# Kernel tuning notes

Hardware: AMD Instinct MI355X
Metric: run time of the kernel (lower is better)

## Reference

```python
import jax, jax.numpy as jnp
import numpy as np

B, T, D = 8, 2048, 256  # batch, time segments, feature dim (a_dim=v_dim=hidden=out=256)
EPS = 1e-8


def _layer_norm(x, g, b, eps=1e-6):
    m = jnp.mean(x, axis=-1, keepdims=True)
    v = jnp.var(x, axis=-1, keepdims=True)
    return (x - m) * jax.lax.rsqrt(v + eps) * g + b


def setup_inputs() -> dict:
    key = jax.random.key(0)
    ks = jax.random.split(key, 9)
    xav = lambda k: jax.random.uniform(k, (D, D), jnp.float32, -1.0, 1.0) * np.sqrt(6.0 / (D + D))
    return {
        "a_fea": jax.random.normal(ks[0], (B, T, D), jnp.float32),
        "v_fea": jax.random.normal(ks[1], (B, T, D), jnp.float32),
        "thr_val": jnp.float32(0.099),
        "Wv1": xav(ks[2]), "Wv2": xav(ks[3]), "Wvfc": xav(ks[4]),
        "Wa1": xav(ks[5]), "Wa2": xav(ks[6]), "Wafc": xav(ks[7]),
        "ln_g": jnp.ones((D,), jnp.float32),
        "ln_b": jnp.zeros((D,), jnp.float32),
    }


def reference(a_fea, v_fea, thr_val, Wv1, Wv2, Wvfc, Wa1, Wa2, Wafc, ln_g, ln_b):
    relu = jax.nn.relu
    # branch projections (dropout is identity at eval); torch Linear: x @ W.T
    v1 = relu(jnp.einsum('btd,hd->bth', v_fea, Wv1))
    v2 = relu(jnp.einsum('btd,hd->bth', v_fea, Wv2))
    a1 = relu(jnp.einsum('btd,hd->bth', a_fea, Wa1))
    a2 = relu(jnp.einsum('btd,hd->bth', a_fea, Wa2))

    d = v2.shape[-1]
    # scaled cross-modal scores, ReLU'd  [B, Tv, Ta]
    beta_va = relu(jnp.einsum('btd,bsd->bts', v2, a1) / jnp.sqrt(jnp.float32(d)))
    # a->v scores taken BEFORE row-normalization of beta_va (as in torch code)
    beta_av = jnp.transpose(beta_va, (0, 2, 1))

    time = beta_va.shape[-1]
    thr = thr_val * 10.0 / time

    # normalize -> threshold sparsify -> renormalize (v attends to a)
    bn_va = beta_va / (jnp.sum(beta_va, axis=-1, keepdims=True) + EPS)
    g_va = jnp.where(bn_va > thr, bn_va, 0.0)
    g_va = g_va / (jnp.sum(g_va, axis=-1, keepdims=True) + EPS)

    # same for a attends to v
    bn_av = beta_av / (jnp.sum(beta_av, axis=-1, keepdims=True) + EPS)
    g_av = jnp.where(bn_av > thr, bn_av, 0.0)
    g_av = g_av / (jnp.sum(g_av, axis=-1, keepdims=True) + EPS)

    # vectorized form of the diagonal selection double-loop (batch element 0)
    pred = (jnp.diagonal(g_av[0]) > 0).astype(jnp.float32)  # [T]

    a_pos = jnp.einsum('bts,bsd->btd', g_va, a2)
    v_psp = v_fea + a_pos
    v_pos = jnp.einsum('bts,bsd->btd', g_av, v1)
    a_psp = a_fea + v_pos

    v_psp = _layer_norm(relu(jnp.einsum('btd,od->bto', v_psp, Wvfc)), ln_g, ln_b)
    a_psp = _layer_norm(relu(jnp.einsum('btd,od->bto', a_psp, Wafc)), ln_g, ln_b)
    a_v_fuse = 0.5 * (v_psp + a_psp)
    return a_v_fuse, v_psp, a_psp, pred
```

## Files before the change

kernel.cpp:

```cpp
#include <hip/hip_runtime.h>
#include <math.h>

#define TT 2048
#define DD 256
#define NBATCH 8
#define EPSF 1e-8f

typedef unsigned short u16;
typedef __attribute__((ext_vector_type(8))) short short8;
typedef __attribute__((ext_vector_type(4))) float f32x4;

__device__ __forceinline__ u16 f2bf(float x) {
    unsigned int u = __builtin_bit_cast(unsigned int, x);
    u += 0x7fffu + ((u >> 16) & 1u);
    return (u16)(u >> 16);
}
__device__ __forceinline__ float bf2f(u16 h) {
    return __builtin_bit_cast(float, (unsigned int)h << 16);
}

__device__ __forceinline__ int frag_dst(int row, int k) {
    return (((row >> 4) * 4 + (k >> 3)) * 16 + (row & 15)) * 8 + (k & 7);
}

__device__ __forceinline__ int swz(int i) { return i ^ ((i >> 2) & 32); }

template<int BR>
__device__ __forceinline__ void stage_tile(const u16* __restrict__ g, u16* s,
                                           int row0, int k0, int ldk, int tid)
{
    #pragma unroll
    for (int i = 0; i < BR / 64; ++i) {
        const int c = tid + 256 * i;
        const int row = c >> 2, q = c & 3;
        *(int4*)(s + swz(frag_dst(row, q * 8))) =
            *(const int4*)(g + (long)(row0 + row) * ldk + k0 + q * 8);
    }
}

__global__ __launch_bounds__(512)
void proj_kernel(const u16* __restrict__ vfh, const u16* __restrict__ vfl,
                 const u16* __restrict__ afh, const u16* __restrict__ afl,
                 const u16* __restrict__ Wsp,
                 u16* __restrict__ v2h, u16* __restrict__ v2l,
                 u16* __restrict__ a1h, u16* __restrict__ a1l,
                 u16* __restrict__ v1T, u16* __restrict__ a2T)
{
    const int zz = blockIdx.z;
    const u16* Ah = (zz == 1 || zz == 3) ? afh : vfh;
    const u16* Al = (zz == 1 || zz == 3) ? afl : vfl;
    const int widx = (zz == 0) ? 2 : (zz == 1) ? 4 : (zz == 2) ? 0 : 6;
    const u16* Bh = Wsp + widx * DD * DD;
    const u16* Bl = Bh + DD * DD;
    const bool split = zz < 2;
    u16* Oh = (zz == 0) ? v2h : a1h;
    u16* Ol = (zz == 0) ? v2l : a1l;
    u16* OT = (zz == 2) ? v1T : a2T;

    __shared__ __align__(16) u16 Ah_s[128 * 32], Al_s[128 * 32];
    __shared__ __align__(16) u16 Bh_s[64 * 32], Bl_s[64 * 32];
    const int m0 = blockIdx.y * 128, n0 = blockIdx.x * 64;
    const int tid = threadIdx.x, lane = tid & 63, w = tid >> 6;
    const int wy = w >> 2, wx = w & 3;
    f32x4 acc[4] = {};

    const int prow = tid >> 2, pq = tid & 3;
    const int dA = swz(frag_dst(prow, pq * 8));
    const u16* gAh = Ah + (long)(m0 + prow) * DD + pq * 8;
    const u16* gAl = Al + (long)(m0 + prow) * DD + pq * 8;
    const int brow = (tid & 255) >> 2, bq = tid & 3;
    const int dB = swz(frag_dst(brow, bq * 8));
    const u16* gB = ((tid < 256) ? Bh : Bl) + (long)(n0 + brow) * DD + bq * 8;
    u16* sB = (tid < 256) ? Bh_s : Bl_s;

    int4 rAh = *(const int4*)(gAh);
    int4 rAl = *(const int4*)(gAl);
    int4 rB  = *(const int4*)(gB);

    for (int k0 = 0; k0 < DD; k0 += 32) {
        *(int4*)(Ah_s + dA) = rAh;
        *(int4*)(Al_s + dA) = rAl;
        *(int4*)(sB + dB)   = rB;
        __syncthreads();
        const int kn = (k0 + 32 < DD) ? k0 + 32 : 0;
        rAh = *(const int4*)(gAh + kn);
        rAl = *(const int4*)(gAl + kn);
        rB  = *(const int4*)(gB + kn);
        short8 ah[4], al[4], bh, bl;
        #pragma unroll
        for (int i = 0; i < 4; ++i) {
            ah[i] = *(const short8*)(Ah_s + swz(((wy * 4 + i) * 64 + lane) * 8));
            al[i] = *(const short8*)(Al_s + swz(((wy * 4 + i) * 64 + lane) * 8));
        }
        bh = *(const short8*)(Bh_s + swz((wx * 64 + lane) * 8));
        bl = *(const short8*)(Bl_s + swz((wx * 64 + lane) * 8));
        #pragma unroll
        for (int i = 0; i < 4; ++i) {
            acc[i] = __builtin_amdgcn_mfma_f32_16x16x32_bf16(ah[i], bl, acc[i], 0, 0, 0);
            acc[i] = __builtin_amdgcn_mfma_f32_16x16x32_bf16(al[i], bh, acc[i], 0, 0, 0);
            acc[i] = __builtin_amdgcn_mfma_f32_16x16x32_bf16(ah[i], bh, acc[i], 0, 0, 0);
        }
        __syncthreads();
    }
    const int quad = lane >> 4, col = lane & 15;
    const int c = n0 + wx * 16 + col;
    #pragma unroll
    for (int i = 0; i < 4; ++i) {
        const int rbase = m0 + wy * 64 + i * 16 + quad * 4;
        if (split) {
            #pragma unroll
            for (int r = 0; r < 4; ++r) {
                const float v = fmaxf(acc[i][r], 0.f);
                const u16 h = f2bf(v);
                Oh[(long)(rbase + r) * DD + c] = h;
                Ol[(long)(rbase + r) * DD + c] = f2bf(v - bf2f(h));
            }
        } else {
            short4 pk;
            pk.x = (short)f2bf(fmaxf(acc[i][0], 0.f));
            pk.y = (short)f2bf(fmaxf(acc[i][1], 0.f));
            pk.z = (short)f2bf(fmaxf(acc[i][2], 0.f));
            pk.w = (short)f2bf(fmaxf(acc[i][3], 0.f));
            const int b = rbase >> 11, t = rbase & (TT - 1);
            *(short4*)(OT + ((long)b * DD + c) * TT + t) = pk;
        }
    }
}

__global__ __launch_bounds__(512)
void score_kernel(const u16* __restrict__ v2h, const u16* __restrict__ v2l,
                  const u16* __restrict__ a1h, const u16* __restrict__ a1l,
                  u16* __restrict__ beta, u16* __restrict__ betaT,
                  float* __restrict__ rs, float* __restrict__ cs)
{
    __shared__ __align__(16) u16 S[128 * 136];
    u16* Ah_s = S;
    u16* Al_s = S + 4096;
    u16* Bh_s = S + 8192;
    u16* Bl_s = S + 12288;
    const int z = blockIdx.z;
    const int m0 = blockIdx.y * 128, n0 = blockIdx.x * 128;
    const int tid = threadIdx.x, lane = tid & 63, w = tid >> 6;
    const int wy = w >> 2, wx = w & 3;
    const long zoff = (long)z * TT * DD;
    f32x4 acc[4][2] = {};

    const int prow = tid >> 2, pq = tid & 3;
    const int d0 = swz(frag_dst(prow, pq * 8));
    const u16* gAh = v2h + zoff + (long)(m0 + prow) * DD + pq * 8;
    const u16* gAl = v2l + zoff + (long)(m0 + prow) * DD + pq * 8;
    const u16* gBh = a1h + zoff + (long)(n0 + prow) * DD + pq * 8;
    const u16* gBl = a1l + zoff + (long)(n0 + prow) * DD + pq * 8;

    int4 rAh = *(const int4*)(gAh);
    int4 rAl = *(const int4*)(gAl);
    int4 rBh = *(const int4*)(gBh);
    int4 rBl = *(const int4*)(gBl);

    for (int k0 = 0; k0 < DD; k0 += 32) {
        *(int4*)(Ah_s + d0) = rAh;
        *(int4*)(Al_s + d0) = rAl;
        *(int4*)(Bh_s + d0) = rBh;
        *(int4*)(Bl_s + d0) = rBl;
        __syncthreads();
        const int kn = (k0 + 32 < DD) ? k0 + 32 : 0;
        rAh = *(const int4*)(gAh + kn);
        rAl = *(const int4*)(gAl + kn);
        rBh = *(const int4*)(gBh + kn);
        rBl = *(const int4*)(gBl + kn);
        short8 ah[4], al[4], bh[2], bl[2];
        #pragma unroll
        for (int i = 0; i < 4; ++i) {
            ah[i] = *(const short8*)(Ah_s + swz(((wy * 4 + i) * 64 + lane) * 8));
            al[i] = *(const short8*)(Al_s + swz(((wy * 4 + i) * 64 + lane) * 8));
        }
        #pragma unroll
        for (int j = 0; j < 2; ++j) {
            bh[j] = *(const short8*)(Bh_s + swz(((wx * 2 + j) * 64 + lane) * 8));
            bl[j] = *(const short8*)(Bl_s + swz(((wx * 2 + j) * 64 + lane) * 8));
        }
        #pragma unroll
        for (int i = 0; i < 4; ++i)
            #pragma unroll
            for (int j = 0; j < 2; ++j) {
                acc[i][j] = __builtin_amdgcn_mfma_f32_16x16x32_bf16(ah[i], bl[j], acc[i][j], 0, 0, 0);
                acc[i][j] = __builtin_amdgcn_mfma_f32_16x16x32_bf16(al[i], bh[j], acc[i][j], 0, 0, 0);
                acc[i][j] = __builtin_amdgcn_mfma_f32_16x16x32_bf16(ah[i], bh[j], acc[i][j], 0, 0, 0);
            }
        __syncthreads();
    }

    const int quad = lane >> 4, col = lane & 15;
    const float scale = 1.f / 16.f;
    #pragma unroll
    for (int i = 0; i < 4; ++i)
        #pragma unroll
        for (int j = 0; j < 2; ++j)
            #pragma unroll
            for (int r = 0; r < 4; ++r)
                acc[i][j][r] = fmaxf(acc[i][j][r] * scale, 0.f);

    #pragma unroll
    for (int i = 0; i < 4; ++i) {
        const int rl = (wy * 4 + i) * 16 + quad * 4;
        #pragma unroll
        for (int j = 0; j < 2; ++j) {
            const int cl = (wx * 2 + j) * 16 + col;
            #pragma unroll
            for (int r = 0; r < 4; ++r)
                S[(rl + r) * 136 + cl] = f2bf(acc[i][j][r]);
        }
    }
    __syncthreads();
    #pragma unroll
    for (int it = 0; it < 4; ++it) {
        const int idx = tid + 512 * it;
        const int rl = idx >> 4, cq = idx & 15;
        const int4 v = *(const int4*)(S + rl * 136 + cq * 8);
        *(int4*)(beta + ((long)z * TT + m0 + rl) * TT + n0 + cq * 8) = v;
    }
    #pragma unroll
    for (int i = 0; i < 4; ++i)
        #pragma unroll
        for (int r = 0; r < 4; ++r) {
            float rp = acc[i][0][r] + acc[i][1][r];
            rp += __shfl_xor(rp, 1); rp += __shfl_xor(rp, 2);
            rp += __shfl_xor(rp, 4); rp += __shfl_xor(rp, 8);
            if (col == 0) {
                const int row = m0 + (wy * 4 + i) * 16 + quad * 4 + r;
                atomicAdd(&rs[(long)z * TT + row], rp);
            }
        }
    #pragma unroll
    for (int j = 0; j < 2; ++j) {
        float cp = 0.f;
        #pragma unroll
        for (int i = 0; i < 4; ++i)
            #pragma unroll
            for (int r = 0; r < 4; ++r) cp += acc[i][j][r];
        cp += __shfl_xor(cp, 16); cp += __shfl_xor(cp, 32);
        if (lane < 16) {
            const int c = n0 + (wx * 2 + j) * 16 + col;
            atomicAdd(&cs[(long)z * TT + c], cp);
        }
    }
    __syncthreads();
    #pragma unroll
    for (int i = 0; i < 4; ++i)
        #pragma unroll
        for (int j = 0; j < 2; ++j) {
            const int cl = (wx * 2 + j) * 16 + col;
            const int rl = (wy * 4 + i) * 16 + quad * 4;
            short4 pk;
            pk.x = (short)f2bf(acc[i][j][0]);
            pk.y = (short)f2bf(acc[i][j][1]);
            pk.z = (short)f2bf(acc[i][j][2]);
            pk.w = (short)f2bf(acc[i][j][3]);
            *(short4*)(S + cl * 136 + rl) = pk;
        }
    __syncthreads();
    #pragma unroll
    for (int it = 0; it < 4; ++it) {
        const int idx = tid + 512 * it;
        const int cl = idx >> 4, tq = idx & 15;
        const int4 v = *(const int4*)(S + cl * 136 + tq * 8);
        *(int4*)(betaT + ((long)z * TT + n0 + cl) * TT + m0 + tq * 8) = v;
    }
}

__global__ __launch_bounds__(512)
void pv_kernel(const u16* __restrict__ beta, const u16* __restrict__ betaT,
               const u16* __restrict__ a2T, const u16* __restrict__ v1T,
               const float* __restrict__ rs, const float* __restrict__ cs,
               const float* __restrict__ thrp,
               u16* __restrict__ yvin, u16* __restrict__ yain)
{
    __shared__ __align__(16) u16 A_s[128 * 32], B_s[256 * 32];
    __shared__ float sthr[128], sA[128], ssum[128];
    const int zz = blockIdx.x;
    const int m0 = blockIdx.y * 128;
    const int z = zz & 7;
    const bool av = zz >= 8;
    const u16* P      = av ? betaT : beta;
    const u16* VT     = av ? v1T : a2T;
    const float* sums = av ? cs : rs;
    u16* outb         = av ? yain : yvin;

    const int tid = threadIdx.x, lane = tid & 63, w = tid >> 6;
    const int wy = w >> 2, wx = w & 3;
    const float thr = thrp[0] * 10.0f / (float)TT;
    if (tid < 128) {
        const float s = sums[(long)z * TT + m0 + tid];
        sA[tid] = s; sthr[tid] = thr * (s + EPSF); ssum[tid] = 0.f;
    }
    __syncthreads();
    f32x4 acc[4][4] = {};
    float rpart = 0.f;
    const int arow = tid >> 2, aq = tid & 3;
    const u16* Pp = P + ((long)z * TT + m0 + arow) * TT + aq * 8;
    const u16* V0 = VT + (long)z * DD * TT + (long)arow * TT + aq * 8;
    const u16* V1 = V0 + (long)128 * TT;
    const int da  = swz(frag_dst(arow, aq * 8));
    const int db1 = swz(frag_dst(arow + 128, aq * 8));

    int4 Ar  = *(const int4*)(Pp);
    int4 Br0 = *(const int4*)(V0);
    int4 Br1 = *(const int4*)(V1);

    for (int k0 = 0; k0 < TT; k0 += 32) {
        union { int4 v; u16 us[8]; } U;
        U.v = Ar;
        const float ct = sthr[arow];
        float ss = 0.f;
        #pragma unroll
        for (int t = 0; t < 8; ++t) {
            const float v = bf2f(U.us[t]);
            if (v > ct) ss += v; else U.us[t] = 0;
        }
        rpart += ss;
        *(int4*)(A_s + da) = U.v;
        *(int4*)(B_s + da) = Br0;
        *(int4*)(B_s + db1) = Br1;
        __syncthreads();
        const int kn = (k0 + 32 < TT) ? (k0 + 32) : k0;
        Ar  = *(const int4*)(Pp + kn);
        Br0 = *(const int4*)(V0 + kn);
        Br1 = *(const int4*)(V1 + kn);
        short8 a[4], b[4];
        #pragma unroll
        for (int i = 0; i < 4; ++i)
            a[i] = *(const short8*)(A_s + swz(((wy * 4 + i) * 64 + lane) * 8));
        #pragma unroll
        for (int j = 0; j < 4; ++j)
            b[j] = *(const short8*)(B_s + swz(((wx * 4 + j) * 64 + lane) * 8));
        #pragma unroll
        for (int i = 0; i < 4; ++i)
            #pragma unroll
            for (int j = 0; j < 4; ++j)
                acc[i][j] = __builtin_amdgcn_mfma_f32_16x16x32_bf16(a[i], b[j], acc[i][j], 0, 0, 0);
        __syncthreads();
    }
    atomicAdd(&ssum[arow], rpart);
    __syncthreads();

    const int quad = lane >> 4, col = lane & 15;
    #pragma unroll
    for (int i = 0; i < 4; ++i)
        #pragma unroll
        for (int j = 0; j < 4; ++j) {
            const int c = (wx * 4 + j) * 16 + col;
            #pragma unroll
            for (int r = 0; r < 4; ++r) {
                const int lrow = (wy * 4 + i) * 16 + quad * 4 + r;
                const int row = m0 + lrow;
                const float inv = 1.0f / (ssum[lrow] + EPSF * (sA[lrow] + EPSF));
                const long oidx = ((long)z * TT + row) * DD + c;
                const float v = acc[i][j][r] * inv + bf2f(outb[oidx]);
                outb[oidx] = f2bf(v);
            }
        }
}

__global__ __launch_bounds__(256)
void fc_kernel(const u16* __restrict__ Ain, const u16* __restrict__ Wb,
               u16* __restrict__ Cb)
{
    const int z = blockIdx.z;
    const u16* A = Ain + (size_t)z * (size_t)NBATCH * TT * DD;
    const u16* B = Wb + (size_t)z * DD * DD;
    u16* C = Cb + (size_t)z * (size_t)NBATCH * TT * DD;
    __shared__ __align__(16) u16 A_s[128 * 32], B_s[64 * 32];
    const int m0 = blockIdx.y * 128, n0 = blockIdx.x * 64;
    const int tid = threadIdx.x, lane = tid & 63, w = tid >> 6;
    const int wy = w >> 1, wx = w & 1;
    f32x4 acc[4][2] = {};
    for (int k0 = 0; k0 < DD; k0 += 32) {
        stage_tile<128>(A, A_s, m0, k0, DD, tid);
        stage_tile<64>(B, B_s, n0, k0, DD, tid);
        __syncthreads();
        short8 a[4], b[2];
        #pragma unroll
        for (int i = 0; i < 4; ++i)
            a[i] = *(const short8*)(A_s + swz(((wy * 4 + i) * 64 + lane) * 8));
        #pragma unroll
        for (int j = 0; j < 2; ++j)
            b[j] = *(const short8*)(B_s + swz(((wx * 2 + j) * 64 + lane) * 8));
        #pragma unroll
        for (int i = 0; i < 4; ++i)
            #pragma unroll
            for (int j = 0; j < 2; ++j)
                acc[i][j] = __builtin_amdgcn_mfma_f32_16x16x32_bf16(a[i], b[j], acc[i][j], 0, 0, 0);
        __syncthreads();
    }
    const int quad = lane >> 4, col = lane & 15;
    #pragma unroll
    for (int i = 0; i < 4; ++i)
        #pragma unroll
        for (int j = 0; j < 2; ++j) {
            const int c = n0 + (wx * 2 + j) * 16 + col;
            #pragma unroll
            for (int r = 0; r < 4; ++r) {
                const int row = m0 + (wy * 4 + i) * 16 + quad * 4 + r;
                C[(long)row * DD + c] = f2bf(fmaxf(acc[i][j][r], 0.f));
            }
        }
}

__global__ __launch_bounds__(256)
void pred_exact(const float* __restrict__ vf, const float* __restrict__ af,
                const float* __restrict__ Wv2, const float* __restrict__ Wa1,
                const float* __restrict__ cs, const float* __restrict__ thrp,
                float* __restrict__ pred)
{
    __shared__ float vs[8][260];
    __shared__ float as_[8][260];
    __shared__ float red[4][8];
    const int t0 = blockIdx.x * 8;
    const int tid = threadIdx.x;
    {
        const int i = tid >> 5, c = (tid & 31) * 8;
        *(float4*)&vs[i][c] = *(const float4*)(vf + (long)(t0 + i) * DD + c);
        *(float4*)&vs[i][c + 4] = *(const float4*)(vf + (long)(t0 + i) * DD + c + 4);
        *(float4*)&as_[i][c] = *(const float4*)(af + (long)(t0 + i) * DD + c);
        *(float4*)&as_[i][c + 4] = *(const float4*)(af + (long)(t0 + i) * DD + c + 4);
    }
    __syncthreads();
    const int j = tid;
    float av[8] = {0.f}, aa[8] = {0.f};
    for (int k = 0; k < DD; k += 4) {
        const float4 wv = *(const float4*)(Wv2 + (long)j * DD + k);
        const float4 wa = *(const float4*)(Wa1 + (long)j * DD + k);
        #pragma unroll
        for (int i = 0; i < 8; ++i) {
            const float4 x = *(const float4*)&vs[i][k];
            av[i] += wv.x * x.x + wv.y * x.y + wv.z * x.z + wv.w * x.w;
            const float4 y = *(const float4*)&as_[i][k];
            aa[i] += wa.x * y.x + wa.y * y.y + wa.z * y.z + wa.w * y.w;
        }
    }
    float p[8];
    #pragma unroll
    for (int i = 0; i < 8; ++i)
        p[i] = fmaxf(av[i], 0.f) * fmaxf(aa[i], 0.f);
    #pragma unroll
    for (int off = 32; off > 0; off >>= 1)
        #pragma unroll
        for (int i = 0; i < 8; ++i) p[i] += __shfl_xor(p[i], off);
    const int lane = tid & 63, wv_ = tid >> 6;
    if (lane == 0)
        #pragma unroll
        for (int i = 0; i < 8; ++i) red[wv_][i] = p[i];
    __syncthreads();
    if (tid < 8) {
        float d = red[0][tid] + red[1][tid] + red[2][tid] + red[3][tid];
        d = fmaxf(d * (1.f / 16.f), 0.f);
        const float thr = thrp[0] * 10.0f / (float)TT;
        pred[t0 + tid] = (d > thr * (cs[t0 + tid] + EPSF)) ? 1.0f : 0.0f;
    }
}

__global__ __launch_bounds__(256)
void split_feat(const float* __restrict__ vf, const float* __restrict__ af,
                u16* __restrict__ vfh, u16* __restrict__ vfl,
                u16* __restrict__ afh, u16* __restrict__ afl,
                u16* __restrict__ vcp, u16* __restrict__ acp)
{
    const long i4 = ((long)blockIdx.x * 256 + threadIdx.x) * 4;
    const float* src = blockIdx.y ? af : vf;
    u16* dh = blockIdx.y ? afh : vfh;
    u16* dl = blockIdx.y ? afl : vfl;
    u16* dc = blockIdx.y ? acp : vcp;
    float4 a = *(const float4*)(src + i4);
    ushort4 h4, l4; u16 h;
    h = f2bf(a.x); h4.x = h; l4.x = f2bf(a.x - bf2f(h));
    h = f2bf(a.y); h4.y = h; l4.y = f2bf(a.y - bf2f(h));
    h = f2bf(a.z); h4.z = h; l4.z = f2bf(a.z - bf2f(h));
    h = f2bf(a.w); h4.w = h; l4.w = f2bf(a.w - bf2f(h));
    *(ushort4*)(dh + i4) = h4;
    *(ushort4*)(dl + i4) = l4;
    *(ushort4*)(dc + i4) = h4;
}

__global__ __launch_bounds__(256)
void split_w(const float* __restrict__ w0, const float* __restrict__ w1,
             const float* __restrict__ w2, const float* __restrict__ w3,
             const float* __restrict__ w4, const float* __restrict__ w5,
             u16* __restrict__ out)
{
    const int t = blockIdx.y;
    const float* w = (t == 0) ? w0 : (t == 1) ? w1 : (t == 2) ? w2
                   : (t == 3) ? w3 : (t == 4) ? w4 : w5;
    const int i4 = (blockIdx.x * 256 + threadIdx.x) * 4;
    float4 a = *(const float4*)(w + i4);
    if (t < 4) {
        u16* oh = out + (size_t)t * 2 * DD * DD;
        u16* ol = oh + DD * DD;
        ushort4 h4, l4; u16 h;
        h = f2bf(a.x); h4.x = h; l4.x = f2bf(a.x - bf2f(h));
        h = f2bf(a.y); h4.y = h; l4.y = f2bf(a.y - bf2f(h));
        h = f2bf(a.z); h4.z = h; l4.z = f2bf(a.z - bf2f(h));
        h = f2bf(a.w); h4.w = h; l4.w = f2bf(a.w - bf2f(h));
        *(ushort4*)(oh + i4) = h4;
        *(ushort4*)(ol + i4) = l4;
    } else {
        u16* ob = out + (size_t)8 * DD * DD + (size_t)(t - 4) * DD * DD;
        ushort4 o;
        o.x = f2bf(a.x); o.y = f2bf(a.y); o.z = f2bf(a.z); o.w = f2bf(a.w);
        *(ushort4*)(ob + i4) = o;
    }
}

__global__ __launch_bounds__(256)
void ln_fuse_kernel(const u16* __restrict__ yv, const u16* __restrict__ ya,
                    const float* __restrict__ g, const float* __restrict__ b,
                    float* __restrict__ fuse, float* __restrict__ vpsp,
                    float* __restrict__ apsp)
{
    const long row = (long)blockIdx.x * 4 + (threadIdx.x >> 6);
    const int lane = threadIdx.x & 63;
    const ushort4 hv = *(const ushort4*)(yv + row * DD + lane * 4);
    const ushort4 ha = *(const ushort4*)(ya + row * DD + lane * 4);
    const float xv0 = bf2f(hv.x), xv1 = bf2f(hv.y), xv2 = bf2f(hv.z), xv3 = bf2f(hv.w);
    const float xa0 = bf2f(ha.x), xa1 = bf2f(ha.y), xa2 = bf2f(ha.z), xa3 = bf2f(ha.w);
    float sv = xv0 + xv1 + xv2 + xv3;
    float sa = xa0 + xa1 + xa2 + xa3;
    #pragma unroll
    for (int off = 32; off > 0; off >>= 1) {
        sv += __shfl_xor(sv, off);
        sa += __shfl_xor(sa, off);
    }
    const float mv = sv * (1.f / 256.f);
    const float ma = sa * (1.f / 256.f);
    const float dv0 = xv0 - mv, dv1 = xv1 - mv, dv2 = xv2 - mv, dv3 = xv3 - mv;
    const float da0 = xa0 - ma, da1 = xa1 - ma, da2 = xa2 - ma, da3 = xa3 - ma;
    float qv = dv0 * dv0 + dv1 * dv1 + dv2 * dv2 + dv3 * dv3;
    float qa = da0 * da0 + da1 * da1 + da2 * da2 + da3 * da3;
    #pragma unroll
    for (int off = 32; off > 0; off >>= 1) {
        qv += __shfl_xor(qv, off);
        qa += __shfl_xor(qa, off);
    }
    const float rv = rsqrtf(qv * (1.f / 256.f) + 1e-6f);
    const float ra = rsqrtf(qa * (1.f / 256.f) + 1e-6f);
    const float4 gg = *(const float4*)(g + lane * 4);
    const float4 bb = *(const float4*)(b + lane * 4);
    float4 ov, oa, of;
    ov.x = dv0 * rv * gg.x + bb.x; ov.y = dv1 * rv * gg.y + bb.y;
    ov.z = dv2 * rv * gg.z + bb.z; ov.w = dv3 * rv * gg.w + bb.w;
    oa.x = da0 * ra * gg.x + bb.x; oa.y = da1 * ra * gg.y + bb.y;
    oa.z = da2 * ra * gg.z + bb.z; oa.w = da3 * ra * gg.w + bb.w;
    of.x = 0.5f * (ov.x + oa.x); of.y = 0.5f * (ov.y + oa.y);
    of.z = 0.5f * (ov.z + oa.z); of.w = 0.5f * (ov.w + oa.w);
    *(float4*)(vpsp + row * DD + lane * 4) = ov;
    *(float4*)(apsp + row * DD + lane * 4) = oa;
    *(float4*)(fuse + row * DD + lane * 4) = of;
}

extern "C" void kernel_launch(void* const* d_in, const int* in_sizes, int n_in,
                              void* d_out, int out_size, void* d_ws, size_t ws_size,
                              hipStream_t stream)
{
    const float* a_fea = (const float*)d_in[0];
    const float* v_fea = (const float*)d_in[1];
    const float* thrp  = (const float*)d_in[2];
    const float* Wv1   = (const float*)d_in[3];
    const float* Wv2   = (const float*)d_in[4];
    const float* Wvfc  = (const float*)d_in[5];
    const float* Wa1   = (const float*)d_in[6];
    const float* Wa2   = (const float*)d_in[7];
    const float* Wafc  = (const float*)d_in[8];
    const float* lng   = (const float*)d_in[9];
    const float* lnb   = (const float*)d_in[10];

    const long MT = (long)NBATCH * TT;
    float* out_fuse = (float*)d_out;
    float* out_vpsp = out_fuse + MT * DD;
    float* out_apsp = out_vpsp + MT * DD;
    float* out_pred = out_apsp + MT * DD;

    char* ws = (char*)d_ws;
    const size_t fb = (size_t)MT * DD * sizeof(u16);
    const size_t sumB = (size_t)MT * sizeof(float);
    u16* v2h  = (u16*)(ws + 0 * fb);
    u16* v2l  = (u16*)(ws + 1 * fb);
    u16* a1h  = (u16*)(ws + 2 * fb);
    u16* a1l  = (u16*)(ws + 3 * fb);
    u16* yvin = (u16*)(ws + 4 * fb);
    u16* yain = (u16*)(ws + 5 * fb);
    u16* v1T  = (u16*)(ws + 6 * fb);
    u16* a2T  = (u16*)(ws + 7 * fb);
    char* p = ws + 8 * fb;
    float* rs = (float*)(p + 0 * sumB);
    float* cs = (float*)(p + 1 * sumB);
    u16* Wsp  = (u16*)(p + 2 * sumB);
    char* q = p + 2 * sumB + 10 * DD * DD * sizeof(u16);
    const size_t betaB = (size_t)NBATCH * TT * TT * sizeof(u16);
    u16* beta  = (u16*)q;
    u16* betaT = (u16*)(q + betaB);
    u16* vfh = (u16*)q;
    u16* vfl = vfh + MT * DD;
    u16* afh = vfl + MT * DD;
    u16* afl = afh + MT * DD;
    u16* yvb = (u16*)(ws + 0 * fb);
    u16* yab = yvb + (size_t)MT * DD;

    hipMemsetAsync(rs, 0, 2 * sumB, stream);

    const dim3 blk(256, 1, 1);

    split_feat<<<dim3((unsigned)(MT * DD / 1024), 2, 1), blk, 0, stream>>>(
        v_fea, a_fea, vfh, vfl, afh, afl, yvin, yain);
    split_w<<<dim3(DD * DD / 1024, 6, 1), blk, 0, stream>>>(
        Wv1, Wv2, Wa1, Wa2, Wvfc, Wafc, Wsp);

    proj_kernel<<<dim3(DD / 64, (unsigned)(MT / 128), 4), dim3(512, 1, 1), 0, stream>>>(
        vfh, vfl, afh, afl, Wsp, v2h, v2l, a1h, a1l, v1T, a2T);

    score_kernel<<<dim3(TT / 128, TT / 128, NBATCH), dim3(512, 1, 1), 0, stream>>>(
        v2h, v2l, a1h, a1l, beta, betaT, rs, cs);
    pred_exact<<<dim3(TT / 8, 1, 1), blk, 0, stream>>>(
        v_fea, a_fea, Wv2, Wa1, cs, thrp, out_pred);

    pv_kernel<<<dim3(2 * NBATCH, TT / 128, 1), dim3(512, 1, 1), 0, stream>>>(
        beta, betaT, a2T, v1T, rs, cs, thrp, yvin, yain);

    fc_kernel<<<dim3(DD / 64, (unsigned)(MT / 128), 2), blk, 0, stream>>>(
        yvin, Wsp + 8 * DD * DD, yvb);
    ln_fuse_kernel<<<dim3((unsigned)(MT / 4), 1, 1), blk, 0, stream>>>(
        yvb, yab, lng, lnb, out_fuse, out_vpsp, out_apsp);
}
```

Baseline: 407.2 us.

## Reorder score tiles by batch, read fp32 residual in pv, register-prefetch fc_kernel

After: 425.7 us. 1.05x slower.

```diff
diff --git a/kernel.cpp b/kernel.cpp
--- a/kernel.cpp
+++ b/kernel.cpp
@@ -138,8 +138,10 @@
     u16* Al_s = S + 4096;
     u16* Bh_s = S + 8192;
     u16* Bl_s = S + 12288;
-    const int z = blockIdx.z;
-    const int m0 = blockIdx.y * 128, n0 = blockIdx.x * 128;
+    const int flat = blockIdx.x + (blockIdx.y << 4) + (blockIdx.z << 8);
+    const int z = flat & 7;
+    const int tile = flat >> 3;
+    const int m0 = (tile >> 4) * 128, n0 = (tile & 15) * 128;
     const int tid = threadIdx.x, lane = tid & 63, w = tid >> 6;
     const int wy = w >> 2, wx = w & 3;
     const long zoff = (long)z * TT * DD;
@@ -273,6 +275,7 @@
                const u16* __restrict__ a2T, const u16* __restrict__ v1T,
                const float* __restrict__ rs, const float* __restrict__ cs,
                const float* __restrict__ thrp,
+               const float* __restrict__ v_fea, const float* __restrict__ a_fea,
                u16* __restrict__ yvin, u16* __restrict__ yain)
 {
     __shared__ __align__(16) u16 A_s[128 * 32], B_s[256 * 32];
@@ -284,6 +287,7 @@
     const u16* P      = av ? betaT : beta;
     const u16* VT     = av ? v1T : a2T;
     const float* sums = av ? cs : rs;
+    const float* resid = av ? a_fea : v_fea;
     u16* outb         = av ? yain : yvin;
 
     const int tid = threadIdx.x, lane = tid & 63, w = tid >> 6;
@@ -354,14 +358,13 @@
                 const int lrow = (wy * 4 + i) * 16 + quad * 4 + r;
                 const int row = m0 + lrow;
                 const float inv = 1.0f / (ssum[lrow] + EPSF * (sA[lrow] + EPSF));
-                const long oidx = ((long)z * TT + row) * DD + c;
-                const float v = acc[i][j][r] * inv + bf2f(outb[oidx]);
-                outb[oidx] = f2bf(v);
+                const float v = acc[i][j][r] * inv + resid[((long)z * TT + row) * DD + c];
+                outb[((long)z * TT + row) * DD + c] = f2bf(v);
             }
         }
 }
 
-__global__ __launch_bounds__(256)
+__global__ __launch_bounds__(512)
 void fc_kernel(const u16* __restrict__ Ain, const u16* __restrict__ Wb,
                u16* __restrict__ Cb)
 {
@@ -372,38 +375,46 @@
     __shared__ __align__(16) u16 A_s[128 * 32], B_s[64 * 32];
     const int m0 = blockIdx.y * 128, n0 = blockIdx.x * 64;
     const int tid = threadIdx.x, lane = tid & 63, w = tid >> 6;
-    const int wy = w >> 1, wx = w & 1;
-    f32x4 acc[4][2] = {};
+    const int wy = w >> 2, wx = w & 3;
+    f32x4 acc[4] = {};
+
+    const int prow = tid >> 2, pq = tid & 3;
+    const int dA = swz(frag_dst(prow, pq * 8));
+    const u16* gA = A + (long)(m0 + prow) * DD + pq * 8;
+    const int brow = (tid & 255) >> 2, bq = tid & 3;
+    const int dB = swz(frag_dst(brow, bq * 8));
+    const u16* gB = B + (long)(n0 + brow) * DD + bq * 8;
+
+    int4 rA = *(const int4*)(gA);
+    int4 rB = *(const int4*)(gB);
+
     for (int k0 = 0; k0 < DD; k0 += 32) {
-        stage_tile<128>(A, A_s, m0, k0, DD, tid);
-        stage_tile<64>(B, B_s, n0, k0, DD, tid);
-        __syncthreads();
-        short8 a[4], b[2];
+        *(int4*)(A_s + dA) = rA;
+        if (tid < 256) *(int4*)(B_s + dB) = rB;
+        __syncthreads();
+        const int kn = (k0 + 32 < DD) ? k0 + 32 : 0;
+        rA = *(const int4*)(gA + kn);
+        rB = *(const int4*)(gB + kn);
+        short8 a[4], b;
         #pragma unroll
         for (int i = 0; i < 4; ++i)
             a[i] = *(const short8*)(A_s + swz(((wy * 4 + i) * 64 + lane) * 8));
-        #pragma unroll
-        for (int j = 0; j < 2; ++j)
-            b[j] = *(const short8*)(B_s + swz(((wx * 2 + j) * 64 + lane) * 8));
+        b = *(const short8*)(B_s + swz((wx * 64 + lane) * 8));
         #pragma unroll
         for (int i = 0; i < 4; ++i)
-            #pragma unroll
-            for (int j = 0; j < 2; ++j)
-                acc[i][j] = __builtin_amdgcn_mfma_f32_16x16x32_bf16(a[i], b[j], acc[i][j], 0, 0, 0);
+            acc[i] = __builtin_amdgcn_mfma_f32_16x16x32_bf16(a[i], b, acc[i], 0, 0, 0);
         __syncthreads();
     }
     const int quad = lane >> 4, col = lane & 15;
-    #pragma unroll
-    for (int i = 0; i < 4; ++i)
-        #pragma unroll
-        for (int j = 0; j < 2; ++j) {
-            const int c = n0 + (wx * 2 + j) * 16 + col;
-            #pragma unroll
-            for (int r = 0; r < 4; ++r) {
-                const int row = m0 + (wy * 4 + i) * 16 + quad * 4 + r;
-                C[(long)row * DD + c] = f2bf(fmaxf(acc[i][j][r], 0.f));
-            }
-        }
+    const int c = n0 + wx * 16 + col;
+    #pragma unroll
+    for (int i = 0; i < 4; ++i) {
+        #pragma unroll
+        for (int r = 0; r < 4; ++r) {
+            const int row = m0 + wy * 64 + i * 16 + quad * 4 + r;
+            C[(long)row * DD + c] = f2bf(fmaxf(acc[i][r], 0.f));
+        }
+    }
 }
 
 __global__ __launch_bounds__(256)
@@ -462,14 +473,12 @@
 __global__ __launch_bounds__(256)
 void split_feat(const float* __restrict__ vf, const float* __restrict__ af,
                 u16* __restrict__ vfh, u16* __restrict__ vfl,
-                u16* __restrict__ afh, u16* __restrict__ afl,
-                u16* __restrict__ vcp, u16* __restrict__ acp)
+                u16* __restrict__ afh, u16* __restrict__ afl)
 {
     const long i4 = ((long)blockIdx.x * 256 + threadIdx.x) * 4;
     const float* src = blockIdx.y ? af : vf;
     u16* dh = blockIdx.y ? afh : vfh;
     u16* dl = blockIdx.y ? afl : vfl;
-    u16* dc = blockIdx.y ? acp : vcp;
     float4 a = *(const float4*)(src + i4);
     ushort4 h4, l4; u16 h;
     h = f2bf(a.x); h4.x = h; l4.x = f2bf(a.x - bf2f(h));
@@ -478,7 +487,6 @@
     h = f2bf(a.w); h4.w = h; l4.w = f2bf(a.w - bf2f(h));
     *(ushort4*)(dh + i4) = h4;
     *(ushort4*)(dl + i4) = l4;
-    *(ushort4*)(dc + i4) = h4;
 }
 
 __global__ __launch_bounds__(256)
@@ -609,7 +617,7 @@
     const dim3 blk(256, 1, 1);
 
     split_feat<<<dim3((unsigned)(MT * DD / 1024), 2, 1), blk, 0, stream>>>(
-        v_fea, a_fea, vfh, vfl, afh, afl, yvin, yain);
+        v_fea, a_fea, vfh, vfl, afh, afl);
     split_w<<<dim3(DD * DD / 1024, 6, 1), blk, 0, stream>>>(
         Wv1, Wv2, Wa1, Wa2, Wvfc, Wafc, Wsp);
 
@@ -622,9 +630,9 @@
         v_fea, a_fea, Wv2, Wa1, cs, thrp, out_pred);
 
     pv_kernel<<<dim3(2 * NBATCH, TT / 128, 1), dim3(512, 1, 1), 0, stream>>>(
-        beta, betaT, a2T, v1T, rs, cs, thrp, yvin, yain);
-
-    fc_kernel<<<dim3(DD / 64, (unsigned)(MT / 128), 2), blk, 0, stream>>>(
+        beta, betaT, a2T, v1T, rs, cs, thrp, v_fea, a_fea, yvin, yain);
+
+    fc_kernel<<<dim3(DD / 64, (unsigned)(MT / 128), 2), dim3(512, 1, 1), 0, stream>>>(
         yvin, Wsp + 8 * DD * DD, yvb);
     ln_fuse_kernel<<<dim3((unsigned)(MT / 4), 1, 1), blk, 0, stream>>>(
         yvb, yab, lng, lnb, out_fuse, out_vpsp, out_apsp);
```
